# Optimization experiments

Measured on AMD Instinct MI355X. Metric: run time of the kernel, lower is better.

## Reference

```python
import jax, jax.numpy as jnp
import numpy as np

IMG_H, IMG_W = 832.0, 1472.0
PATCH = 32
NUM_CLASSES = 4
LAMBDA_BOX = 5.0
LAMBDA_CLS = 1.0
B, N, T = 512, 1176, 64


def setup_inputs() -> dict:
    key = jax.random.key(0)
    k1, k2, k3, k4, k5, k6 = jax.random.split(key, 6)
    predictions = jax.random.normal(k1, (B, N, 5 + NUM_CLASSES), dtype=jnp.float32)
    # build valid absolute-pixel target boxes (x1 < x2, y1 < y2)
    x1 = jax.random.uniform(k2, (B, T), dtype=jnp.float32) * (IMG_W - 260.0)
    y1 = jax.random.uniform(k3, (B, T), dtype=jnp.float32) * (IMG_H - 260.0)
    w = 16.0 + jax.random.uniform(k4, (B, T), dtype=jnp.float32) * 240.0
    h = 16.0 + jax.random.uniform(k5, (B, T), dtype=jnp.float32) * 240.0
    target_boxes = jnp.stack([x1, y1, x1 + w, y1 + h], axis=-1)  # (B,T,4)
    target_classes = jax.random.randint(k6, (B, T), 0, NUM_CLASSES, dtype=jnp.int32)
    return {"predictions": predictions, "target_boxes": target_boxes,
            "target_classes": target_classes}


def _decode_boxes(pred):
    # pred: (B,N,9) -> absolute corner boxes (B,N,4)
    cx = (pred[..., 0] * 2.0 - 1.0) * (IMG_W / 2.0)
    cy = (pred[..., 1] * 2.0 - 1.0) * (IMG_H / 2.0)
    w = jnp.exp(pred[..., 2]) * (IMG_W / (IMG_W // PATCH))  # stride 32
    h = jnp.exp(pred[..., 3]) * (IMG_H / (IMG_H // PATCH))
    return jnp.stack([cx - w / 2, cy - h / 2, cx + w / 2, cy + h / 2], axis=-1)


def _pairwise_iou(boxes, tgt):
    # boxes: (B,N,4), tgt: (B,T,4) -> (B,N,T)
    b = boxes[:, :, None, :]
    t = tgt[:, None, :, :]
    ix1 = jnp.maximum(b[..., 0], t[..., 0])
    iy1 = jnp.maximum(b[..., 1], t[..., 1])
    ix2 = jnp.minimum(b[..., 2], t[..., 2])
    iy2 = jnp.minimum(b[..., 3], t[..., 3])
    inter = jnp.maximum(ix2 - ix1, 0.0) * jnp.maximum(iy2 - iy1, 0.0)
    a1 = (b[..., 2] - b[..., 0]) * (b[..., 3] - b[..., 1])
    a2 = (t[..., 2] - t[..., 0]) * (t[..., 3] - t[..., 1])
    union = a1 + a2 - inter
    return jnp.where(union > 0, inter / jnp.where(union > 0, union, 1.0), 0.0)


def _smooth_l1_sum(a, b):
    d = jnp.abs(a - b)
    return jnp.sum(jnp.where(d < 1.0, 0.5 * d * d, d - 0.5))


def _bce_logits_sum(logits, targets):
    # sum of max(x,0) - x*t + log(1+exp(-|x|)) == logaddexp(0,x) - x*t
    return jnp.sum(jnp.logaddexp(0.0, logits) - logits * targets)


def reference(predictions, target_boxes, target_classes):
    batch = predictions.shape[0]
    boxes = _decode_boxes(predictions)                      # (B,N,4)
    ious = _pairwise_iou(jax.lax.stop_gradient(boxes), target_boxes)  # (B,N,T)
    matched = jnp.argmax(ious, axis=1)                      # (B,T) indices into N

    # positive mask via scatter (mirrors positive_mask[matched_preds] = True)
    batch_idx = jnp.arange(batch)[:, None]
    pos = jnp.zeros((batch, boxes.shape[1]), jnp.float32).at[batch_idx, matched].set(1.0)

    # box loss (SmoothL1, sum)
    pred_matched = jnp.take_along_axis(boxes, matched[..., None], axis=1)  # (B,T,4)
    box_loss = _smooth_l1_sum(pred_matched, target_boxes)

    # class loss (CrossEntropy, sum)
    cls_logits_all = predictions[..., 5:5 + NUM_CLASSES]    # (B,N,C)
    cls_logits = jnp.take_along_axis(
        cls_logits_all, matched[..., None], axis=1)          # (B,T,C)
    logp = jax.nn.log_softmax(cls_logits, axis=-1)
    cls_loss = -jnp.sum(jnp.take_along_axis(
        logp, target_classes[..., None].astype(jnp.int32), axis=-1))

    # confidence loss (BCEWithLogits, sum) over all predictions
    conf_loss = _bce_logits_sum(predictions[..., 4], pos)

    total = LAMBDA_BOX * box_loss + LAMBDA_CLS * cls_loss + conf_loss
    return total / batch
```

## Files before the change

### kernel.cpp

```cpp
#include <hip/hip_runtime.h>

#define BATCH   512
#define NPRED   1176
#define NTGT    64
#define PRED_C  9
#define THREADS 512
#define NWAVE   8
#define WCHUNK  147
#define SEGCAP  148
#define NMASKW  ((NPRED + 31) / 32)
#define INVALID 0xFFFF

__device__ __forceinline__ float fexp(float x)  { return __expf(x); }
__device__ __forceinline__ float flog(float x)  { return __logf(x); }

__global__ __launch_bounds__(THREADS) void det_loss_main(
    const float* __restrict__ pred,
    const float* __restrict__ tbox,
    const int*   __restrict__ tcls,
    float* __restrict__ partial)
{
    __shared__ float4 cbox[NWAVE * SEGCAP];
    __shared__ float  carea[NWAVE * SEGCAP];
    __shared__ unsigned short cidx[NWAVE * SEGCAP];
    __shared__ float4 stgt[NTGT];
    __shared__ float  slogit[NPRED];
    __shared__ unsigned int smask[NMASKW];
    __shared__ float  sbint[THREADS];
    __shared__ float  sbuni[THREADS];
    __shared__ unsigned short sbslot[THREADS];
    __shared__ float  shull[4];
    __shared__ float  sred[NWAVE];

    const int b   = blockIdx.x;
    const int tid = threadIdx.x;
    const int wv  = tid >> 6, ln = tid & 63;
    const float* pb = pred + (size_t)b * NPRED * PRED_C;

    if (tid < NMASKW) smask[tid] = 0u;

    if (tid < NTGT) {
        float4 tb = *reinterpret_cast<const float4*>(
            tbox + ((size_t)b * NTGT + tid) * 4);
        stgt[tid] = tb;
        float x1 = tb.x, y1 = tb.y, x2 = tb.z, y2 = tb.w;
        for (int off = 32; off > 0; off >>= 1) {
            x1 = fminf(x1, __shfl_xor(x1, off));
            y1 = fminf(y1, __shfl_xor(y1, off));
            x2 = fmaxf(x2, __shfl_xor(x2, off));
            y2 = fmaxf(y2, __shfl_xor(y2, off));
        }
        if (tid == 0) {
            shull[0] = x1; shull[1] = y1; shull[2] = x2; shull[3] = y2;
        }
    }
    __syncthreads();

    const float hx1 = shull[0], hy1 = shull[1];
    const float hx2 = shull[2], hy2 = shull[3];

    float s_conf = 0.f;
    int wcount = 0;
    const int n0 = wv * WCHUNK;
    for (int i = 0; i < 3; ++i) {
        int r = i * 64 + ln;
        int n = n0 + r;
        bool keep = false;
        float4 bb; float area = 0.f;
        if (r < WCHUNK) {
            const float* p = pb + n * PRED_C;
            float p0 = p[0], p1 = p[1], p2 = p[2], p3 = p[3], p4 = p[4];
            float cx = (p0 * 2.f - 1.f) * 736.f;
            float cy = (p1 * 2.f - 1.f) * 416.f;
            float w  = fexp(p2) * 32.f;
            float h  = fexp(p3) * 32.f;
            bb = make_float4(cx - 0.5f * w, cy - 0.5f * h,
                             cx + 0.5f * w, cy + 0.5f * h);
            area = w * h;
            slogit[n] = p4;
            s_conf += fmaxf(p4, 0.f) + flog(1.f + fexp(-fabsf(p4)));
            keep = (bb.x < hx2) & (bb.z > hx1) & (bb.y < hy2) & (bb.w > hy1);
        }
        unsigned long long m = __ballot(keep);
        if (keep) {
            int pos  = wcount + __popcll(m & ((1ull << ln) - 1ull));
            int slot = wv * SEGCAP + pos;
            cbox[slot]  = bb;
            carea[slot] = area;
            cidx[slot]  = (unsigned short)n;
        }
        wcount += __popcll(m);
    }
    __syncthreads();

    {
        float4 tb = stgt[ln];
        float a2 = (tb.z - tb.x) * (tb.w - tb.y);
        float binter = 0.f, buni = 1.f;
        int   bslot = INVALID;
        const int base = wv * SEGCAP;
        for (int j = 0; j < wcount; ++j) {
            float4 bb = cbox[base + j];
            float a1  = carea[base + j];
            float ix1 = fmaxf(bb.x, tb.x);
            float iy1 = fmaxf(bb.y, tb.y);
            float ix2 = fminf(bb.z, tb.z);
            float iy2 = fminf(bb.w, tb.w);
            float iw  = fmaxf(ix2 - ix1, 0.f);
            float ih  = fmaxf(iy2 - iy1, 0.f);
            float inter = iw * ih;
            float uni   = (a1 + a2) - inter;
            bool better = inter * buni > binter * uni;
            binter = better ? inter : binter;
            buni   = better ? uni   : buni;
            bslot  = better ? (base + j) : bslot;
        }
        sbint[tid] = binter; sbuni[tid] = buni;
        sbslot[tid] = (unsigned short)bslot;
    }
    __syncthreads();

    float s_box = 0.f, s_cls = 0.f;
    if (tid < NTGT) {
        float binter = sbint[tid], buni = sbuni[tid];
        int   bslot = sbslot[tid];
        for (int w = 1; w < NWAVE; ++w) {
            float ci = sbint[w * 64 + tid];
            float cu = sbuni[w * 64 + tid];
            bool better = ci * buni > binter * cu;
            binter = better ? ci : binter;
            buni   = better ? cu : buni;
            bslot  = better ? sbslot[w * 64 + tid] : bslot;
        }
        int m; float4 pbx;
        if (bslot == INVALID) {
            m = 0;
            float p0 = pb[0], p1 = pb[1], p2 = pb[2], p3 = pb[3];
            float cx = (p0 * 2.f - 1.f) * 736.f;
            float cy = (p1 * 2.f - 1.f) * 416.f;
            float w  = fexp(p2) * 32.f;
            float h  = fexp(p3) * 32.f;
            pbx = make_float4(cx - 0.5f * w, cy - 0.5f * h,
                              cx + 0.5f * w, cy + 0.5f * h);
        } else {
            m = cidx[bslot];
            pbx = cbox[bslot];
        }
        atomicOr(&smask[m >> 5], 1u << (m & 31));

        float4 tb = stgt[tid];
        float d;
        d = fabsf(pbx.x - tb.x); s_box += (d < 1.f) ? 0.5f * d * d : d - 0.5f;
        d = fabsf(pbx.y - tb.y); s_box += (d < 1.f) ? 0.5f * d * d : d - 0.5f;
        d = fabsf(pbx.z - tb.z); s_box += (d < 1.f) ? 0.5f * d * d : d - 0.5f;
        d = fabsf(pbx.w - tb.w); s_box += (d < 1.f) ? 0.5f * d * d : d - 0.5f;

        const float* pc = pb + m * PRED_C + 5;
        float x0 = pc[0], x1 = pc[1], x2 = pc[2], x3 = pc[3];
        float mx = fmaxf(fmaxf(x0, x1), fmaxf(x2, x3));
        float se = fexp(x0 - mx) + fexp(x1 - mx) + fexp(x2 - mx) + fexp(x3 - mx);
        float lse = mx + flog(se);
        int tc = tcls[(size_t)b * NTGT + tid];
        float xt = (tc == 0) ? x0 : (tc == 1) ? x1 : (tc == 2) ? x2 : x3;
        s_cls += lse - xt;
    }
    __syncthreads();

    float s_pos = 0.f;
    for (int n = tid; n < NPRED; n += THREADS)
        if (smask[n >> 5] & (1u << (n & 31))) s_pos += slogit[n];

    float v = s_conf - s_pos + 5.f * s_box + s_cls;
    for (int off = 32; off > 0; off >>= 1)
        v += __shfl_down(v, off);
    if (ln == 0) sred[wv] = v;
    __syncthreads();
    if (tid == 0) {
        float t = 0.f;
        for (int i = 0; i < NWAVE; ++i) t += sred[i];
        partial[b] = t;
    }
}

__global__ __launch_bounds__(BATCH) void det_loss_final(
    const float* __restrict__ partial, float* __restrict__ out)
{
    int tid = threadIdx.x;
    float v = partial[tid];
    for (int off = 32; off > 0; off >>= 1)
        v += __shfl_down(v, off);
    __shared__ float s[8];
    if ((tid & 63) == 0) s[tid >> 6] = v;
    __syncthreads();
    if (tid == 0) {
        float t = 0.f;
        for (int i = 0; i < 8; ++i) t += s[i];
        *out = t * (1.f / BATCH);
    }
}

extern "C" void kernel_launch(void* const* d_in, const int* in_sizes, int n_in,
                              void* d_out, int out_size, void* d_ws, size_t ws_size,
                              hipStream_t stream) {
    const float* pred = (const float*)d_in[0];
    const float* tbox = (const float*)d_in[1];
    const int*   tcls = (const int*)d_in[2];
    float* out     = (float*)d_out;
    float* partial = (float*)d_ws;

    det_loss_main<<<BATCH, THREADS, 0, stream>>>(pred, tbox, tcls, partial);
    det_loss_final<<<1, BATCH, 0, stream>>>(partial, out);
}
```

Baseline: 13.10 us.

## Split each batch's predictions across two blocks and add a merge kernel

The main kernel now launches two blocks per batch, each handling half of the 1176 predictions. Each block writes per-target best IoU candidates (intersection, union, index) and its confidence partial sum to workspace. A new 64-thread kernel merges the two halves, recomputes the matched box, computes the box and class losses, and sums positive logits using a bitmask. The intent is to double block-level parallelism and shorten the per-block critical path. In exchange it adds a kernel launch, workspace round-trips, and a tie-break between halves that may differ from argmax-first order. One block-wide barrier is replaced by a wave-local waitcnt.

```diff
diff --git a/kernel.cpp b/kernel.cpp
--- a/kernel.cpp
+++ b/kernel.cpp
@@ -2,42 +2,39 @@
 
 #define BATCH   512
 #define NPRED   1176
+#define HALF    588
 #define NTGT    64
 #define PRED_C  9
 #define THREADS 512
 #define NWAVE   8
-#define WCHUNK  147
-#define SEGCAP  148
-#define NMASKW  ((NPRED + 31) / 32)
-#define INVALID 0xFFFF
+#define SEGCAP  76
+#define NMASKW  37
+#define INVALID_S 0xFFFFu
+#define INVALID_U 0xFFFFFFFFu
 
 __device__ __forceinline__ float fexp(float x)  { return __expf(x); }
 __device__ __forceinline__ float flog(float x)  { return __logf(x); }
 
-__global__ __launch_bounds__(THREADS) void det_loss_main(
+__global__ __launch_bounds__(THREADS) void det_k1(
     const float* __restrict__ pred,
     const float* __restrict__ tbox,
-    const int*   __restrict__ tcls,
-    float* __restrict__ partial)
+    float2* __restrict__ iu,
+    unsigned int* __restrict__ idxb,
+    float* __restrict__ bce)
 {
     __shared__ float4 cbox[NWAVE * SEGCAP];
     __shared__ float  carea[NWAVE * SEGCAP];
     __shared__ unsigned short cidx[NWAVE * SEGCAP];
     __shared__ float4 stgt[NTGT];
-    __shared__ float  slogit[NPRED];
-    __shared__ unsigned int smask[NMASKW];
     __shared__ float  sbint[THREADS];
     __shared__ float  sbuni[THREADS];
     __shared__ unsigned short sbslot[THREADS];
     __shared__ float  shull[4];
     __shared__ float  sred[NWAVE];
 
-    const int b   = blockIdx.x;
-    const int tid = threadIdx.x;
-    const int wv  = tid >> 6, ln = tid & 63;
+    const int bh  = blockIdx.x, b = bh >> 1, h = bh & 1;
+    const int tid = threadIdx.x, wv = tid >> 6, ln = tid & 63;
     const float* pb = pred + (size_t)b * NPRED * PRED_C;
-
-    if (tid < NMASKW) smask[tid] = 0u;
 
     if (tid < NTGT) {
         float4 tb = *reinterpret_cast<const float4*>(
@@ -59,25 +56,26 @@
     const float hx1 = shull[0], hy1 = shull[1];
     const float hx2 = shull[2], hy2 = shull[3];
 
+    const int lo = h * HALF + (wv * HALF) / NWAVE;
+    const int hi = h * HALF + ((wv + 1) * HALF) / NWAVE;
+    const int cnt = hi - lo;
     float s_conf = 0.f;
     int wcount = 0;
-    const int n0 = wv * WCHUNK;
-    for (int i = 0; i < 3; ++i) {
+    for (int i = 0; i < 2; ++i) {
         int r = i * 64 + ln;
-        int n = n0 + r;
+        int n = lo + r;
         bool keep = false;
         float4 bb; float area = 0.f;
-        if (r < WCHUNK) {
+        if (r < cnt) {
             const float* p = pb + n * PRED_C;
             float p0 = p[0], p1 = p[1], p2 = p[2], p3 = p[3], p4 = p[4];
             float cx = (p0 * 2.f - 1.f) * 736.f;
             float cy = (p1 * 2.f - 1.f) * 416.f;
             float w  = fexp(p2) * 32.f;
-            float h  = fexp(p3) * 32.f;
-            bb = make_float4(cx - 0.5f * w, cy - 0.5f * h,
-                             cx + 0.5f * w, cy + 0.5f * h);
-            area = w * h;
-            slogit[n] = p4;
+            float hh = fexp(p3) * 32.f;
+            bb = make_float4(cx - 0.5f * w, cy - 0.5f * hh,
+                             cx + 0.5f * w, cy + 0.5f * hh);
+            area = w * hh;
             s_conf += fmaxf(p4, 0.f) + flog(1.f + fexp(-fabsf(p4)));
             keep = (bb.x < hx2) & (bb.z > hx1) & (bb.y < hy2) & (bb.w > hy1);
         }
@@ -91,13 +89,13 @@
         }
         wcount += __popcll(m);
     }
-    __syncthreads();
+    asm volatile("s_waitcnt lgkmcnt(0)" ::: "memory");
 
     {
         float4 tb = stgt[ln];
         float a2 = (tb.z - tb.x) * (tb.w - tb.y);
         float binter = 0.f, buni = 1.f;
-        int   bslot = INVALID;
+        int   bslot = INVALID_S;
         const int base = wv * SEGCAP;
         for (int j = 0; j < wcount; ++j) {
             float4 bb = cbox[base + j];
@@ -120,7 +118,6 @@
     }
     __syncthreads();
 
-    float s_box = 0.f, s_cls = 0.f;
     if (tid < NTGT) {
         float binter = sbint[tid], buni = sbuni[tid];
         int   bslot = sbslot[tid];
@@ -132,45 +129,13 @@
             buni   = better ? cu : buni;
             bslot  = better ? sbslot[w * 64 + tid] : bslot;
         }
-        int m; float4 pbx;
-        if (bslot == INVALID) {
-            m = 0;
-            float p0 = pb[0], p1 = pb[1], p2 = pb[2], p3 = pb[3];
-            float cx = (p0 * 2.f - 1.f) * 736.f;
-            float cy = (p1 * 2.f - 1.f) * 416.f;
-            float w  = fexp(p2) * 32.f;
-            float h  = fexp(p3) * 32.f;
-            pbx = make_float4(cx - 0.5f * w, cy - 0.5f * h,
-                              cx + 0.5f * w, cy + 0.5f * h);
-        } else {
-            m = cidx[bslot];
-            pbx = cbox[bslot];
-        }
-        atomicOr(&smask[m >> 5], 1u << (m & 31));
-
-        float4 tb = stgt[tid];
-        float d;
-        d = fabsf(pbx.x - tb.x); s_box += (d < 1.f) ? 0.5f * d * d : d - 0.5f;
-        d = fabsf(pbx.y - tb.y); s_box += (d < 1.f) ? 0.5f * d * d : d - 0.5f;
-        d = fabsf(pbx.z - tb.z); s_box += (d < 1.f) ? 0.5f * d * d : d - 0.5f;
-        d = fabsf(pbx.w - tb.w); s_box += (d < 1.f) ? 0.5f * d * d : d - 0.5f;
-
-        const float* pc = pb + m * PRED_C + 5;
-        float x0 = pc[0], x1 = pc[1], x2 = pc[2], x3 = pc[3];
-        float mx = fmaxf(fmaxf(x0, x1), fmaxf(x2, x3));
-        float se = fexp(x0 - mx) + fexp(x1 - mx) + fexp(x2 - mx) + fexp(x3 - mx);
-        float lse = mx + flog(se);
-        int tc = tcls[(size_t)b * NTGT + tid];
-        float xt = (tc == 0) ? x0 : (tc == 1) ? x1 : (tc == 2) ? x2 : x3;
-        s_cls += lse - xt;
-    }
-    __syncthreads();
-
-    float s_pos = 0.f;
-    for (int n = tid; n < NPRED; n += THREADS)
-        if (smask[n >> 5] & (1u << (n & 31))) s_pos += slogit[n];
-
-    float v = s_conf - s_pos + 5.f * s_box + s_cls;
+        unsigned int n = (bslot == (int)INVALID_S) ? INVALID_U
+                                                   : (unsigned int)cidx[bslot];
+        iu[(size_t)bh * NTGT + tid]   = make_float2(binter, buni);
+        idxb[(size_t)bh * NTGT + tid] = n;
+    }
+
+    float v = s_conf;
     for (int off = 32; off > 0; off >>= 1)
         v += __shfl_down(v, off);
     if (ln == 0) sred[wv] = v;
@@ -178,11 +143,79 @@
     if (tid == 0) {
         float t = 0.f;
         for (int i = 0; i < NWAVE; ++i) t += sred[i];
-        partial[b] = t;
-    }
-}
-
-__global__ __launch_bounds__(BATCH) void det_loss_final(
+        bce[bh] = t;
+    }
+}
+
+__global__ __launch_bounds__(64) void det_k2(
+    const float* __restrict__ pred,
+    const float* __restrict__ tbox,
+    const int*   __restrict__ tcls,
+    const float2* __restrict__ iu,
+    const unsigned int* __restrict__ idxb,
+    const float* __restrict__ bce,
+    float* __restrict__ partial)
+{
+    __shared__ unsigned int smask[NMASKW];
+    const int b = blockIdx.x, t = threadIdx.x;
+    if (t < NMASKW) smask[t] = 0u;
+
+    float2 a0 = iu[((size_t)b * 2 + 0) * NTGT + t];
+    float2 a1 = iu[((size_t)b * 2 + 1) * NTGT + t];
+    unsigned int n0 = idxb[((size_t)b * 2 + 0) * NTGT + t];
+    unsigned int n1 = idxb[((size_t)b * 2 + 1) * NTGT + t];
+    bool better = a1.x * a0.y > a0.x * a1.y;
+    unsigned int n = better ? n1 : n0;
+    const int m = (n == INVALID_U) ? 0 : (int)n;
+
+    __syncthreads();
+    atomicOr(&smask[m >> 5], 1u << (m & 31));
+
+    const float* pm = pred + (size_t)b * NPRED * PRED_C + m * PRED_C;
+    float p0 = pm[0], p1 = pm[1], p2 = pm[2], p3 = pm[3];
+    float cx = (p0 * 2.f - 1.f) * 736.f;
+    float cy = (p1 * 2.f - 1.f) * 416.f;
+    float w  = fexp(p2) * 32.f;
+    float hh = fexp(p3) * 32.f;
+    float bx1 = cx - 0.5f * w, by1 = cy - 0.5f * hh;
+    float bx2 = cx + 0.5f * w, by2 = cy + 0.5f * hh;
+
+    float4 tb = *reinterpret_cast<const float4*>(
+        tbox + ((size_t)b * NTGT + t) * 4);
+    float s_box = 0.f, d;
+    d = fabsf(bx1 - tb.x); s_box += (d < 1.f) ? 0.5f * d * d : d - 0.5f;
+    d = fabsf(by1 - tb.y); s_box += (d < 1.f) ? 0.5f * d * d : d - 0.5f;
+    d = fabsf(bx2 - tb.z); s_box += (d < 1.f) ? 0.5f * d * d : d - 0.5f;
+    d = fabsf(by2 - tb.w); s_box += (d < 1.f) ? 0.5f * d * d : d - 0.5f;
+
+    float x0 = pm[5], x1 = pm[6], x2 = pm[7], x3 = pm[8];
+    float mx = fmaxf(fmaxf(x0, x1), fmaxf(x2, x3));
+    float se = fexp(x0 - mx) + fexp(x1 - mx) + fexp(x2 - mx) + fexp(x3 - mx);
+    float lse = mx + flog(se);
+    int tc = tcls[(size_t)b * NTGT + t];
+    float xt = (tc == 0) ? x0 : (tc == 1) ? x1 : (tc == 2) ? x2 : x3;
+    float s_cls = lse - xt;
+
+    __syncthreads();
+
+    float s_pos = 0.f;
+    if (t < NMASKW) {
+        unsigned int mw = smask[t];
+        while (mw) {
+            int bit = __ffs(mw) - 1; mw &= mw - 1;
+            int mm = t * 32 + bit;
+            s_pos += pred[(size_t)b * NPRED * PRED_C + mm * PRED_C + 4];
+        }
+    }
+
+    float v = 5.f * s_box + s_cls - s_pos;
+    if (t == 0) v += bce[(size_t)b * 2] + bce[(size_t)b * 2 + 1];
+    for (int off = 32; off > 0; off >>= 1)
+        v += __shfl_down(v, off);
+    if (t == 0) partial[b] = v;
+}
+
+__global__ __launch_bounds__(BATCH) void det_k3(
     const float* __restrict__ partial, float* __restrict__ out)
 {
     int tid = threadIdx.x;
@@ -205,9 +238,14 @@
     const float* pred = (const float*)d_in[0];
     const float* tbox = (const float*)d_in[1];
     const int*   tcls = (const int*)d_in[2];
-    float* out     = (float*)d_out;
-    float* partial = (float*)d_ws;
-
-    det_loss_main<<<BATCH, THREADS, 0, stream>>>(pred, tbox, tcls, partial);
-    det_loss_final<<<1, BATCH, 0, stream>>>(partial, out);
-}
+    float* out = (float*)d_out;
+
+    float2*       iu      = (float2*)d_ws;
+    unsigned int* idxb    = (unsigned int*)((char*)d_ws + 524288);
+    float*        bce     = (float*)((char*)d_ws + 786432);
+    float*        partial = (float*)((char*)d_ws + 790528);
+
+    det_k1<<<2 * BATCH, THREADS, 0, stream>>>(pred, tbox, iu, idxb, bce);
+    det_k2<<<BATCH, 64, 0, stream>>>(pred, tbox, tcls, iu, idxb, bce, partial);
+    det_k3<<<1, BATCH, 0, stream>>>(partial, out);
+}
```

Result: slower. 16.11 us (+23.0%).
